# Kernel tuning notes

Measured on AMD Instinct MI355X. Metric: run time of the kernel, lower is better.

Reference implementation:

```python
import jax, jax.numpy as jnp
import numpy as np

EPS = 1e-12  # F.normalize eps

def _l2norm(v, axis):
    n = jnp.sqrt(jnp.sum(v * v, axis=axis, keepdims=True))
    return v / jnp.maximum(n, EPS)

def setup_inputs() -> dict:
    key = jax.random.key(0)
    k1, k2, k3, k4 = jax.random.split(key, 4)
    B, C, H, W, K = 8, 1024, 64, 64, 64
    x = jax.random.normal(k1, (B, C, H, W), dtype=jnp.float32)
    centroids = jax.random.normal(k2, (K, C), dtype=jnp.float32)
    # 1x1 conv initialized to identity in the module; use random perturbed weights for a non-trivial test
    fc_weight = jax.random.normal(k3, (C, C), dtype=jnp.float32) * 0.02 + jnp.eye(C, dtype=jnp.float32)
    fc_bias = jax.random.normal(k4, (C,), dtype=jnp.float32) * 0.01
    return {"x": x, "centroids": centroids, "fc_weight": fc_weight, "fc_bias": fc_bias}

def reference(x, centroids, fc_weight, fc_bias):
    B, C, H, W = x.shape
    K = centroids.shape[0]
    # Eq.1: nearest-centroid assignment via cosine similarity
    x_n = _l2norm(x, axis=1)            # [B,C,H,W]
    g_n = _l2norm(centroids, axis=1)    # [K,C]
    sim = jnp.einsum('bchw,nc->bnhw', x_n, g_n)          # [B,K,H,W]
    idx = jnp.argmax(sim, axis=1)                        # [B,H,W]
    assign = jax.nn.one_hot(idx, K, dtype=x.dtype)       # [B,H,W,K]
    # Eq.2: batch-wise local centroids
    sum_x = jnp.einsum('bhwn,bchw->bnc', assign, x)      # [B,K,C]
    count = jnp.sum(assign, axis=(1, 2))[..., None]      # [B,K,1]
    centroids_local = sum_x / jnp.maximum(count, 1.0)    # [B,K,C]
    # Eq.3,4: calibration
    lk_map = jnp.einsum('bhwn,bnc->bchw', assign, centroids_local)  # [B,C,H,W]
    delta = lk_map - x
    w = jnp.exp(-jnp.mean(delta * delta, axis=1, keepdims=True))    # [B,1,H,W]
    x_cal = x + w * delta
    # 1x1 conv + relu
    out = jnp.einsum('oc,bchw->bohw', fc_weight, x_cal) + fc_bias[None, :, None, None]
    return jax.nn.relu(out)
```

## Files before the change

kernel.cpp:

```cpp
#include <hip/hip_runtime.h>
#include <stdint.h>

#define B_   8
#define C_   1024
#define HW_  4096
#define K_   64
#define NPIX (B_*HW_)
#define SLAB ((size_t)B_*K_*C_)
#define NSEG 8

typedef __attribute__((ext_vector_type(8))) short short8;
typedef __attribute__((ext_vector_type(4))) float f32x4;

__device__ __forceinline__ uint16_t f2bf(float f) {
  uint32_t u = __float_as_uint(f);
  u += 0x7fffu + ((u >> 16) & 1u);
  return (uint16_t)(u >> 16);
}

__device__ __forceinline__ void gl2lds16(const uint16_t* g, uint16_t* l) {
  __builtin_amdgcn_global_load_lds(
      (const __attribute__((address_space(1))) unsigned int*)(g),
      (__attribute__((address_space(3))) unsigned int*)(l), 16, 0, 0);
}

__global__ void prep_gT(const float* __restrict__ g, float* __restrict__ gT) {
  int n = blockIdx.x;
  int t = threadIdx.x;
  float vals[4]; float ss = 0.f;
  #pragma unroll
  for (int i = 0; i < 4; i++) { float v = g[n*C_ + t + i*256]; vals[i] = v; ss += v*v; }
  __shared__ float red[256];
  red[t] = ss; __syncthreads();
  for (int s = 128; s > 0; s >>= 1) { if (t < s) red[t] += red[t+s]; __syncthreads(); }
  float scale = 1.f / fmaxf(sqrtf(red[0]), 1e-12f);
  #pragma unroll
  for (int i = 0; i < 4; i++) gT[(t + i*256)*K_ + n] = vals[i]*scale;
}

__global__ void prep_wb(const float* __restrict__ w, uint16_t* __restrict__ wb) {
  int i = blockIdx.x*256 + threadIdx.x;
  float4 v = *(const float4*)&w[i*4];
  uint16_t o[4] = {f2bf(v.x), f2bf(v.y), f2bf(v.z), f2bf(v.w)};
  *(uint64_t*)&wb[i*4] = *(const uint64_t*)o;
}

__launch_bounds__(256)
__global__ void pass_assign(const float* __restrict__ x, const float* __restrict__ gT,
                            int* __restrict__ idx, int* __restrict__ count) {
  int bb = blockIdx.x >> 6;
  int pt = blockIdx.x & 63;
  int t = threadIdx.x;
  int lane = t & 63;
  int w = t >> 6;
  int ng = __builtin_amdgcn_readfirstlane(w);
  __shared__ alignas(16) float xs[2][32][64];
  const float* xb = x + (size_t)bb*C_*HW_ + pt*64;
  const float* gp = gT + ng*16;

  int r0 = t >> 4;
  int q0 = t & 15;
  const float* p0 = xb + (size_t)r0*HW_ + q0*4;
  const float* p1 = p0 + (size_t)16*HW_;

  float acc[16];
  #pragma unroll
  for (int n = 0; n < 16; n++) acc[n] = 0.f;

  {
    float4 v0 = *(const float4*)p0;
    float4 v1 = *(const float4*)p1;
    *(float4*)&xs[0][r0][q0*4]    = v0;
    *(float4*)&xs[0][r0+16][q0*4] = v1;
  }
  __syncthreads();
  for (int cc = 0; cc < 32; cc++) {
    int cur = cc & 1;
    float4 n0, n1;
    if (cc + 1 < 32) {
      n0 = *(const float4*)(p0 + (size_t)(cc + 1)*32*HW_);
      n1 = *(const float4*)(p1 + (size_t)(cc + 1)*32*HW_);
    }
    #pragma unroll 16
    for (int ci = 0; ci < 32; ci++) {
      float xv = xs[cur][ci][lane];
      const float* gr = gp + (cc*32 + ci)*K_;
      #pragma unroll
      for (int n2 = 0; n2 < 16; n2++) acc[n2] = fmaf(xv, gr[n2], acc[n2]);
    }
    if (cc + 1 < 32) {
      *(float4*)&xs[cur^1][r0][q0*4]    = n0;
      *(float4*)&xs[cur^1][r0+16][q0*4] = n1;
    }
    __syncthreads();
  }

  float best = acc[0]; int bi = 0;
  #pragma unroll
  for (int n = 1; n < 16; n++) { if (acc[n] > best) { best = acc[n]; bi = n; } }
  __shared__ float bv[4][64];
  __shared__ int   bn[4][64];
  __shared__ int   hist[64];
  if (t < 64) hist[t] = 0;
  bv[w][lane] = best; bn[w][lane] = ng*16 + bi;
  __syncthreads();
  if (t < 64) {
    float mv = bv[0][t]; int mn = bn[0][t];
    #pragma unroll
    for (int wv2 = 1; wv2 < 4; wv2++) { if (bv[wv2][t] > mv) { mv = bv[wv2][t]; mn = bn[wv2][t]; } }
    idx[bb*HW_ + pt*64 + t] = mn;
    atomicAdd(&hist[mn], 1);
  }
  __syncthreads();
  if (t < 64 && hist[t] > 0) atomicAdd(&count[bb*K_ + t], hist[t]);
}

__launch_bounds__(256)
__global__ void pass_bins(const float* __restrict__ x, const int* __restrict__ idx,
                          float* __restrict__ sumxp) {
  int bid = blockIdx.x;
  int ps = bid & 7;
  int ct = (bid >> 3) & 15;
  int bb = bid >> 7;
  int t = threadIdx.x;
  int lane = t & 63;
  int w = t >> 6;
  int col = lane & 15;
  int kg  = lane >> 4;
  int crow = ct*64 + w*16 + col;
  const float* xp = x + (size_t)bb*C_*HW_ + (size_t)crow*HW_ + ps*512 + kg*8;
  const int*   ip = idx + bb*HW_ + ps*512 + kg*8;

  const f32x4 fzero = {0.f, 0.f, 0.f, 0.f};
  f32x4 acc[4];
  #pragma unroll
  for (int f = 0; f < 4; f++) acc[f] = fzero;

  for (int ks = 0; ks < 16; ks++) {
    float a0[8];
    *(float4*)&a0[0] = *(const float4*)&xp[ks*32];
    *(float4*)&a0[4] = *(const float4*)&xp[ks*32 + 4];
    short8 af;
    #pragma unroll
    for (int j = 0; j < 8; j++) af[j] = (short)f2bf(a0[j]);
    int iv8[8];
    *(int4*)&iv8[0] = *(const int4*)&ip[ks*32];
    *(int4*)&iv8[4] = *(const int4*)&ip[ks*32 + 4];
    #pragma unroll
    for (int f = 0; f < 4; f++) {
      int n = f*16 + col;
      short8 bfrag;
      #pragma unroll
      for (int j = 0; j < 8; j++) bfrag[j] = (short)((iv8[j] == n) ? 0x3F80 : 0);
      acc[f] = __builtin_amdgcn_mfma_f32_16x16x32_bf16(af, bfrag, acc[f], 0, 0, 0);
    }
  }
  #pragma unroll
  for (int f = 0; f < 4; f++) {
    int n = f*16 + col;
    size_t base = (size_t)ps*SLAB + ((size_t)bb*K_ + n)*C_ + ct*64 + w*16 + kg*4;
    *(f32x4*)&sumxp[base] = acc[f];
  }
}

__launch_bounds__(256)
__global__ void pass_cfinal(const float* __restrict__ sumxp, const int* __restrict__ count,
                            float* __restrict__ cl, float* __restrict__ clT,
                            float* __restrict__ cn2) {
  int bb = blockIdx.x >> 6, n = blockIdx.x & 63, t = threadIdx.x;
  float inv = 1.f / fmaxf((float)count[bb*K_ + n], 1.f);
  float ss = 0.f;
  #pragma unroll
  for (int i = 0; i < 4; i++) {
    int c = t + i*256;
    size_t o = ((size_t)bb*K_ + n)*C_ + c;
    float v = 0.f;
    #pragma unroll
    for (int s = 0; s < NSEG; s++) v += sumxp[o + (size_t)s*SLAB];
    v *= inv;
    cl [((size_t)bb*K_ + n)*C_ + c] = v;
    clT[((size_t)bb*C_ + c)*K_ + n] = v;
    ss += v*v;
  }
  __shared__ float red[256];
  red[t] = ss; __syncthreads();
  for (int s = 128; s > 0; s >>= 1) { if (t < s) red[t] += red[t+s]; __syncthreads(); }
  if (t == 0) cn2[bb*K_ + n] = red[0];
}

__launch_bounds__(256)
__global__ void pass_xcal(const float* __restrict__ x, const int* __restrict__ idx,
                          const float* __restrict__ cl, const float* __restrict__ clT,
                          const float* __restrict__ cn2, uint16_t* __restrict__ xcal) {
  int bb = blockIdx.x >> 6, pt = blockIdx.x & 63, t = threadIdx.x;
  int lane = t & 63, cs = t >> 6;
  __shared__ float xT[64][129];
  __shared__ int   widx[64];
  __shared__ float pdot[4][64], pxsq[4][64], wv[64];
  if (t < 64) widx[t] = idx[bb*HW_ + pt*64 + t];
  __syncthreads();
  const float* xb = x + (size_t)bb*C_*HW_ + pt*64;
  int myi = widx[lane];
  const float* clb = clT + (size_t)bb*C_*K_ + myi;
  float dp = 0.f, xq = 0.f;
  #pragma unroll 4
  for (int ci = 0; ci < 256; ci++) {
    int c = cs*256 + ci;
    float xv = xb[(size_t)c*HW_ + lane];
    dp = fmaf(xv, clb[(size_t)c*K_], dp);
    xq = fmaf(xv, xv, xq);
  }
  pdot[cs][lane] = dp; pxsq[cs][lane] = xq;
  __syncthreads();
  if (t < 64) {
    float d = pdot[0][t]+pdot[1][t]+pdot[2][t]+pdot[3][t];
    float q = pxsq[0][t]+pxsq[1][t]+pxsq[2][t]+pxsq[3][t];
    float msd = (q - 2.f*d + cn2[bb*K_ + widx[t]]) * (1.f/1024.f);
    wv[t] = expf(-msd);
  }
  __syncthreads();
  for (int cc = 0; cc < 8; cc++) {
    #pragma unroll
    for (int i = 0; i < 32; i++) {
      int co = cs*32 + i;
      xT[lane][co] = xb[(size_t)(cc*128 + co)*HW_ + lane];
    }
    __syncthreads();
    #pragma unroll 2
    for (int pp = 0; pp < 16; pp++) {
      int p = pp*4 + cs;
      float wval = wv[p]; int iv = widx[p];
      const float* clr = cl + ((size_t)bb*K_ + iv)*C_ + cc*128;
      size_t obase = ((size_t)(bb*HW_ + pt*64 + p))*C_ + cc*128;
      #pragma unroll
      for (int ci = 0; ci < 2; ci++) {
        int co = ci*64 + lane;
        float xvv = xT[p][co];
        float v = fmaf(wval, clr[co] - xvv, xvv);
        xcal[obase + co] = f2bf(v);
      }
    }
    __syncthreads();
  }
}

#define BK 64
__launch_bounds__(256)
__global__ void gemm_out(const uint16_t* __restrict__ wb, const uint16_t* __restrict__ xcal,
                         const float* __restrict__ bias, float* __restrict__ out) {
  __shared__ alignas(16) uint16_t smem[2*2*128*BK];
  float* ep = (float*)smem;
  int t = threadIdx.x;
  int lane = t & 63;
  int w = t >> 6, wm = w & 1, wn = w >> 1;
  int g  = blockIdx.x & 7;
  int li = blockIdx.x >> 3;
  int ot = li & 7;
  int qt = g*32 + (li >> 3);

  const uint16_t* wsrc = wb   + (size_t)ot*128*C_;
  const uint16_t* xsrc = xcal + (size_t)qt*128*C_;

  const f32x4 fzero = {0.f, 0.f, 0.f, 0.f};
  f32x4 acc[4][4];
  #pragma unroll
  for (int i = 0; i < 4; i++)
    #pragma unroll
    for (int j = 0; j < 4; j++) acc[i][j] = fzero;

  auto STAGE = [&](int buf, int kb) {
    uint16_t* lw = smem + (size_t)buf*2*128*BK;
    uint16_t* lx = lw + 128*BK;
    #pragma unroll
    for (int it = 0; it < 4; it++) {
      int s = t + it*256;
      int r = s >> 3, q = s & 7;
      int qm = q ^ (r & 7);
      uint16_t* ldw = lw + (size_t)(it*256 + w*64)*8;
      uint16_t* ldx = lx + (size_t)(it*256 + w*64)*8;
      gl2lds16(wsrc + (size_t)r*C_ + kb*BK + qm*8, ldw);
      gl2lds16(xsrc + (size_t)r*C_ + kb*BK + qm*8, ldx);
    }
  };

  STAGE(0, 0);
  __syncthreads();
  for (int kb = 0; kb < C_/BK; kb++) {
    int cur = kb & 1;
    if (kb + 1 < C_/BK) STAGE(cur ^ 1, kb + 1);
    const uint16_t* lw = smem + (size_t)cur*2*128*BK;
    const uint16_t* lx = lw + 128*BK;
    #pragma unroll
    for (int kk = 0; kk < 2; kk++) {
      short8 af[4], bf[4];
      #pragma unroll
      for (int i = 0; i < 4; i++) {
        int row = wm*64 + i*16 + (lane & 15);
        int q = kk*4 + (lane >> 4);
        af[i] = *(const short8*)&lw[row*BK + (q ^ (row & 7))*8];
      }
      #pragma unroll
      for (int j = 0; j < 4; j++) {
        int row = wn*64 + j*16 + (lane & 15);
        int q = kk*4 + (lane >> 4);
        bf[j] = *(const short8*)&lx[row*BK + (q ^ (row & 7))*8];
      }
      #pragma unroll
      for (int i = 0; i < 4; i++)
        #pragma unroll
        for (int j = 0; j < 4; j++)
          acc[i][j] = __builtin_amdgcn_mfma_f32_16x16x32_bf16(af[i], bf[j], acc[i][j], 0, 0, 0);
    }
    __syncthreads();
  }
  int col = lane & 15, quad = lane >> 4;
  int bq = (qt*128) >> 12;
  int p0 = (qt*128) & 4095;
  #pragma unroll
  for (int ph = 0; ph < 2; ph++) {
    if (wm == ph) {
      #pragma unroll
      for (int i = 0; i < 4; i++)
        #pragma unroll
        for (int j = 0; j < 4; j++) {
          int p = wn*64 + j*16 + col;
          #pragma unroll
          for (int r = 0; r < 4; r++) {
            int o2 = i*16 + quad*4 + r;
            ep[o2*128 + (((p >> 2) ^ (o2 & 7)) << 2) + (p & 3)] = acc[i][j][r];
          }
        }
    }
    __syncthreads();
    #pragma unroll
    for (int i2 = 0; i2 < 8; i2++) {
      int s = t + i2*256;
      int ol = s >> 5, pf = s & 31;
      float4 v = *(const float4*)&ep[ol*128 + ((pf ^ (ol & 7)) << 2)];
      int o = ot*128 + ph*64 + ol;
      float bi = bias[o];
      v.x = fmaxf(v.x + bi, 0.f); v.y = fmaxf(v.y + bi, 0.f);
      v.z = fmaxf(v.z + bi, 0.f); v.w = fmaxf(v.w + bi, 0.f);
      *(float4*)&out[(size_t)bq*C_*HW_ + (size_t)o*HW_ + p0 + pf*4] = v;
    }
    __syncthreads();
  }
}

extern "C" void kernel_launch(void* const* d_in, const int* in_sizes, int n_in,
                              void* d_out, int out_size, void* d_ws, size_t ws_size,
                              hipStream_t stream) {
  (void)in_sizes; (void)n_in; (void)out_size; (void)ws_size;
  const float* x    = (const float*)d_in[0];
  const float* cent = (const float*)d_in[1];
  const float* fw   = (const float*)d_in[2];
  const float* fb   = (const float*)d_in[3];
  float* out = (float*)d_out;
  char* ws = (char*)d_ws;
  size_t off = 0;
  float*    gT    = (float*)(ws + off);    off += (size_t)C_*K_*4;
  int*      idx   = (int*)(ws + off);      off += (size_t)NPIX*4;
  int*      count = (int*)(ws + off);      off += (size_t)B_*K_*4;
  float*    sumx  = (float*)(ws + off);    off += (size_t)B_*K_*C_*4;
  float*    cl    = (float*)(ws + off);    off += (size_t)B_*K_*C_*4;
  float*    clT   = (float*)(ws + off);    off += (size_t)B_*C_*K_*4;
  float*    cn2   = (float*)(ws + off);    off += (size_t)B_*K_*4 + 8;
  uint16_t* wb    = (uint16_t*)(ws + off); off += (size_t)C_*C_*2;
  uint16_t* xcal  = (uint16_t*)(ws + off); off += (size_t)NPIX*C_*2;
  (void)sumx;
  float* sumxp = (float*)xcal;

  hipMemsetAsync(count, 0, (size_t)B_*K_*4, stream);
  prep_gT   <<<64,   256, 0, stream>>>(cent, gT);
  prep_wb   <<<1024, 256, 0, stream>>>(fw, wb);
  pass_assign<<<512, 256, 0, stream>>>(x, gT, idx, count);
  pass_bins <<<1024, 256, 0, stream>>>(x, idx, sumxp);
  pass_cfinal<<<512, 256, 0, stream>>>(sumxp, count, cl, clT, cn2);
  pass_xcal <<<512,  256, 0, stream>>>(x, idx, cl, clT, cn2, xcal);
  gemm_out  <<<2048, 256, 0, stream>>>(wb, xcal, fb, out);
}
```

Measured before the change: 492.8 us.

## Triple-buffer GEMM K-loop with BK=32 and vmcnt-based partial waits

Changes the output GEMM from double-buffered BK=64 tiles to triple-buffered BK=32 tiles loaded via global_load_lds, prefetching two stages ahead. It replaces the full __syncthreads with explicit s_waitcnt vmcnt(4) plus s_barrier, so in-flight loads for the next stage are not drained each iteration. The aim is to hide global memory latency better while using less LDS. The trade-off is a barrier every 32 K elements instead of every 64, with fewer MFMAs between barriers, and the swizzle narrows from 8 to 4 chunks per row, which may raise LDS bank conflicts.

```diff
diff --git a/kernel.cpp b/kernel.cpp
--- a/kernel.cpp
+++ b/kernel.cpp
@@ -244,11 +244,11 @@
   }
 }
 
-#define BK 64
+#define BK2 32
 __launch_bounds__(256)
 __global__ void gemm_out(const uint16_t* __restrict__ wb, const uint16_t* __restrict__ xcal,
                          const float* __restrict__ bias, float* __restrict__ out) {
-  __shared__ alignas(16) uint16_t smem[2*2*128*BK];
+  __shared__ alignas(16) uint16_t smem[3*2*128*BK2];
   float* ep = (float*)smem;
   int t = threadIdx.x;
   int lane = t & 63;
@@ -269,50 +269,58 @@
     for (int j = 0; j < 4; j++) acc[i][j] = fzero;
 
   auto STAGE = [&](int buf, int kb) {
-    uint16_t* lw = smem + (size_t)buf*2*128*BK;
-    uint16_t* lx = lw + 128*BK;
-    #pragma unroll
-    for (int it = 0; it < 4; it++) {
+    uint16_t* lw = smem + (size_t)buf*2*128*BK2;
+    uint16_t* lx = lw + 128*BK2;
+    #pragma unroll
+    for (int it = 0; it < 2; it++) {
       int s = t + it*256;
-      int r = s >> 3, q = s & 7;
-      int qm = q ^ (r & 7);
+      int r = s >> 2, q = s & 3;
+      int qm = q ^ (r & 3);
       uint16_t* ldw = lw + (size_t)(it*256 + w*64)*8;
       uint16_t* ldx = lx + (size_t)(it*256 + w*64)*8;
-      gl2lds16(wsrc + (size_t)r*C_ + kb*BK + qm*8, ldw);
-      gl2lds16(xsrc + (size_t)r*C_ + kb*BK + qm*8, ldx);
+      gl2lds16(wsrc + (size_t)r*C_ + kb*BK2 + qm*8, ldw);
+      gl2lds16(xsrc + (size_t)r*C_ + kb*BK2 + qm*8, ldx);
     }
   };
 
   STAGE(0, 0);
-  __syncthreads();
-  for (int kb = 0; kb < C_/BK; kb++) {
-    int cur = kb & 1;
-    if (kb + 1 < C_/BK) STAGE(cur ^ 1, kb + 1);
-    const uint16_t* lw = smem + (size_t)cur*2*128*BK;
-    const uint16_t* lx = lw + 128*BK;
-    #pragma unroll
-    for (int kk = 0; kk < 2; kk++) {
-      short8 af[4], bf[4];
-      #pragma unroll
-      for (int i = 0; i < 4; i++) {
-        int row = wm*64 + i*16 + (lane & 15);
-        int q = kk*4 + (lane >> 4);
-        af[i] = *(const short8*)&lw[row*BK + (q ^ (row & 7))*8];
-      }
-      #pragma unroll
-      for (int j = 0; j < 4; j++) {
-        int row = wn*64 + j*16 + (lane & 15);
-        int q = kk*4 + (lane >> 4);
-        bf[j] = *(const short8*)&lx[row*BK + (q ^ (row & 7))*8];
-      }
-      #pragma unroll
-      for (int i = 0; i < 4; i++)
-        #pragma unroll
-        for (int j = 0; j < 4; j++)
-          acc[i][j] = __builtin_amdgcn_mfma_f32_16x16x32_bf16(af[i], bf[j], acc[i][j], 0, 0, 0);
-    }
-    __syncthreads();
-  }
+  STAGE(1, 1);
+  asm volatile("s_waitcnt vmcnt(4)" ::: "memory");
+  __builtin_amdgcn_s_barrier();
+  __builtin_amdgcn_sched_barrier(0);
+
+  for (int kb = 0; kb < C_/BK2; kb++) {
+    int buf = kb % 3;
+    if (kb + 2 < C_/BK2) STAGE((kb + 2) % 3, kb + 2);
+    const uint16_t* lw = smem + (size_t)buf*2*128*BK2;
+    const uint16_t* lx = lw + 128*BK2;
+    short8 af[4], bf[4];
+    #pragma unroll
+    for (int i = 0; i < 4; i++) {
+      int row = wm*64 + i*16 + (lane & 15);
+      int q = lane >> 4;
+      af[i] = *(const short8*)&lw[row*BK2 + (q ^ (row & 3))*8];
+    }
+    #pragma unroll
+    for (int j = 0; j < 4; j++) {
+      int row = wn*64 + j*16 + (lane & 15);
+      int q = lane >> 4;
+      bf[j] = *(const short8*)&lx[row*BK2 + (q ^ (row & 3))*8];
+    }
+    #pragma unroll
+    for (int i = 0; i < 4; i++)
+      #pragma unroll
+      for (int j = 0; j < 4; j++)
+        acc[i][j] = __builtin_amdgcn_mfma_f32_16x16x32_bf16(af[i], bf[j], acc[i][j], 0, 0, 0);
+    if (kb < C_/BK2 - 1) {
+      if (kb + 2 < C_/BK2) asm volatile("s_waitcnt vmcnt(4)" ::: "memory");
+      else                 asm volatile("s_waitcnt vmcnt(0)" ::: "memory");
+      __builtin_amdgcn_s_barrier();
+      __builtin_amdgcn_sched_barrier(0);
+    }
+  }
+  __syncthreads();
+
   int col = lane & 15, quad = lane >> 4;
   int bq = (qt*128) >> 12;
   int p0 = (qt*128) & 4095;
```

Measured after the change: 509.9 us. 3.5% more time.
